# Performance work log

Measured on AMD Instinct MI355X. Metric: run time of the kernel, lower is better.

## Reference

```python
import jax, jax.numpy as jnp
import numpy as np

N, E, D, H, G, L, EF = 50000, 800000, 128, 256, 512, 3, 8
BN_EPS = 1e-5


def _bn(h, g, b):
    # torch BatchNorm1d in training mode: biased batch stats over the node axis
    m = h.mean(0)
    v = h.var(0)
    return g * (h - m) * jax.lax.rsqrt(v + BN_EPS) + b


def setup_inputs() -> dict:
    ks = jax.random.split(jax.random.key(0), 12)
    sc = 0.05
    return {
        "x": jax.random.normal(ks[0], (N, D), jnp.float32),
        "edge_attr": jax.random.normal(ks[1], (E, EF), jnp.float32),
        "vn_emb": jnp.zeros((1, D), jnp.float32),  # init.constant_(0)
        "We": jax.random.normal(ks[2], (L, EF, D)) * sc,
        "be": jnp.zeros((L, D)),
        "W1": jax.random.normal(ks[3], (L, D, H)) * sc,
        "b1": jnp.zeros((L, H)),
        "g1": jnp.ones((L, H)),
        "bt1": jnp.zeros((L, H)),
        "W2": jax.random.normal(ks[4], (L, H, D)) * sc,
        "b2": jnp.zeros((L, D)),
        "gb": jnp.ones((L, D)),
        "bb": jnp.zeros((L, D)),
        "Wv1": jax.random.normal(ks[5], (L - 1, D, H)) * sc,
        "bv1": jnp.zeros((L - 1, H)),
        "gv1": jnp.ones((L - 1, H)),
        "btv1": jnp.zeros((L - 1, H)),
        "Wv2": jax.random.normal(ks[6], (L - 1, H, D)) * sc,
        "bv2": jnp.zeros((L - 1, D)),
        "gv2": jnp.ones((L - 1, D)),
        "btv2": jnp.zeros((L - 1, D)),
        "edge_index": jax.random.randint(ks[7], (2, E), 0, N),
        "batch": jnp.sort(jax.random.randint(ks[8], (N,), 0, G)),
    }


def reference(x, edge_attr, vn_emb, We, be, W1, b1, g1, bt1, W2, b2, gb, bb,
              Wv1, bv1, gv1, btv1, Wv2, bv2, gv2, btv2, edge_index, batch):
    src, dst = edge_index[0], edge_index[1]
    vn = jnp.broadcast_to(vn_emb, (G, D))  # Embedding(1, D) looked up for every graph
    h = x  # node_encoder is None -> encoded_node = x
    for l in range(L):
        h_in = h + vn[batch]                              # virtual-node broadcast (gather)
        e = edge_attr @ We[l] + be[l]                     # per-layer edge encoder
        msg = jax.nn.relu(h_in[src] + e)                  # GIN message, [E, D]
        aggr = jax.ops.segment_sum(msg, dst, num_segments=N)
        z = h_in + aggr                                   # (1+eps)*h + aggr, eps=0
        z = jax.nn.relu(_bn(z @ W1[l] + b1[l], g1[l], bt1[l]))
        h = _bn(z @ W2[l] + b2[l], gb[l], bb[l])          # conv MLP out + outer BatchNorm
        if l < L - 1:
            h = jax.nn.relu(h)                            # dropout ratio 0 -> identity
            pooled = jax.ops.segment_sum(h_in, batch, num_segments=G) + vn
            t = jax.nn.relu(_bn(pooled @ Wv1[l] + bv1[l], gv1[l], btv1[l]))
            vn = jax.nn.relu(_bn(t @ Wv2[l] + bv2[l], gv2[l], btv2[l]))
    return h  # JK == 'last'
```

## Files before the change

kernel.cpp:

```cpp
#include <hip/hip_runtime.h>
#include <hip/hip_bf16.h>

#define N_NODES 50000
#define N_EDGES 800000
#define DIM 128
#define HID 256
#define N_GRAPH 512
#define N_LAYER 3
#define EFEAT 8
#define BN_EPS 1e-5f

typedef unsigned short u16;
typedef unsigned int u32;

using bf16x8_t = short __attribute__((ext_vector_type(8)));
using f32x4_t  = float __attribute__((ext_vector_type(4)));
using f32x2    = float __attribute__((ext_vector_type(2)));


__device__ __forceinline__ void atomic_add_f(float* p, float v) {
    unsafeAtomicAdd(p, v);
}
__device__ __forceinline__ u16 f2bf(float x) {
    union { float f; u32 u; } v; v.f = x;
    u32 r = v.u + 0x7FFF + ((v.u >> 16) & 1);
    return (u16)(r >> 16);
}
__device__ __forceinline__ float bf2f(u16 u) {
    union { u32 i; float f; } v; v.i = (u32)u << 16; return v.f;
}
__device__ __forceinline__ float2 up2(u32 p) {
    return make_float2(bf2f((u16)(p & 0xFFFF)), bf2f((u16)(p >> 16)));
}
__device__ __forceinline__ u32 pk2(float a, float b) {
    return (u32)f2bf(a) | ((u32)f2bf(b) << 16);
}
__device__ __forceinline__ float bflo(u32 u) {
    union { u32 i; float f; } v; v.i = u << 16; return v.f;
}
__device__ __forceinline__ float bfhi(u32 u) {
    union { u32 i; float f; } v; v.i = u & 0xFFFF0000u; return v.f;
}
__device__ __forceinline__ f32x2 up2p(u32 p) {
    union { u32 u[2]; f32x2 f; } v;
    v.u[0] = p << 16;
    v.u[1] = p & 0xFFFF0000u;
    return v.f;
}
__device__ __forceinline__ f32x2 splat2(float x) {
    f32x2 r; r.x = x; r.y = x; return r;
}

__global__ __launch_bounds__(256) void wconv_kernel(
    const float* __restrict__ W1, const float* __restrict__ W2,
    u16* __restrict__ W1t, u16* __restrict__ W2t)
{
    int idx = blockIdx.x * 256 + threadIdx.x;
    if (idx >= 6 * 32768) return;
    int m = idx >> 15;
    int off = idx & 32767;
    int l = m >> 1;
    if ((m & 1) == 0) {
        int r = off >> 8, c = off & 255;
        W1t[(size_t)l * 32768 + c * 128 + r] = f2bf(W1[(size_t)l * 32768 + r * 256 + c]);
    } else {
        int r = off >> 7, c = off & 127;
        W2t[(size_t)l * 32768 + c * 256 + r] = f2bf(W2[(size_t)l * 32768 + r * 128 + c]);
    }
}

__global__ __launch_bounds__(256) void hist_kernel(const int* __restrict__ ei, int* __restrict__ deg) {
    int e = blockIdx.x * 256 + threadIdx.x;
    if (e < N_EDGES) atomicAdd(&deg[ei[N_EDGES + e]], 1);
}

__global__ __launch_bounds__(1024) void scan_kernel(const int* __restrict__ deg, int* __restrict__ rowptr) {
    __shared__ int wsum[16];
    __shared__ int carry;
    int tid = threadIdx.x;
    if (tid == 0) { carry = 0; rowptr[0] = 0; }
    __syncthreads();
    for (int base = 0; base < N_NODES; base += 1024) {
        int i = base + tid;
        int v = (i < N_NODES) ? deg[i] : 0;
        int lane = tid & 63, w = tid >> 6;
        int s = v;
        #pragma unroll
        for (int d = 1; d < 64; d <<= 1) { int t = __shfl_up(s, d); if (lane >= d) s += t; }
        if (lane == 63) wsum[w] = s;
        __syncthreads();
        if (tid < 64) {
            int t = (tid < 16) ? wsum[tid] : 0;
            #pragma unroll
            for (int d = 1; d < 16; d <<= 1) { int u = __shfl_up(t, d); if (tid >= d) t += u; }
            if (tid < 16) wsum[tid] = t;
        }
        __syncthreads();
        int excl = (w > 0) ? wsum[w - 1] : 0;
        int incl = s + excl + carry;
        if (i < N_NODES) rowptr[i + 1] = incl;
        __syncthreads();
        if (tid == 0) carry += wsum[15];
        __syncthreads();
    }
}

__global__ __launch_bounds__(256) void scatter_kernel(
    const int* __restrict__ ei, const float* __restrict__ ea,
    const int* __restrict__ rowptr,
    int* __restrict__ cursor, u32* __restrict__ srcOff, uint4* __restrict__ eabs)
{
    int e = blockIdx.x * 256 + threadIdx.x;
    if (e >= N_EDGES) return;
    int src = ei[e];
    int dst = ei[N_EDGES + e];
    int p = atomicAdd(&cursor[dst], 1);
    int pos = rowptr[dst] + p;
    srcOff[pos] = (u32)src << 8;
    const float4 lo = *(const float4*)(ea + (size_t)e * EFEAT);
    const float4 hi = *(const float4*)(ea + (size_t)e * EFEAT + 4);
    uint4 q;
    q.x = pk2(lo.x, lo.y); q.y = pk2(lo.z, lo.w);
    q.z = pk2(hi.x, hi.y); q.w = pk2(hi.z, hi.w);
    eabs[pos] = q;
}

template <bool USEBN, int VNM>
__global__ __launch_bounds__(256) void hin_kernel(
    const float* __restrict__ src,
    const float* __restrict__ sum2, const float* __restrict__ ss2,
    const float* __restrict__ g, const float* __restrict__ b, float invN,
    const int* __restrict__ batch,
    const float* __restrict__ vn_emb,
    const float* __restrict__ vnpre, const float* __restrict__ vsum, const float* __restrict__ vss,
    const float* __restrict__ gv, const float* __restrict__ btv, float invG,
    u16* __restrict__ hin, int total4)
{
    int idx = blockIdx.x * 256 + threadIdx.x;
    if (idx >= total4) return;
    int base = idx * 4;
    int n = base >> 7;
    int c = base & (DIM - 1);
    float4 v = *(const float4*)(src + base);
    float o[4] = {v.x, v.y, v.z, v.w};
    if (USEBN) {
        #pragma unroll
        for (int j = 0; j < 4; ++j) {
            int cj = c + j;
            float m = sum2[cj] * invN;
            float var = ss2[cj] * invN - m * m;
            float r = rsqrtf(var + BN_EPS);
            float a = g[cj] * r;
            o[j] = fmaxf(fmaf(a, o[j], b[cj] - m * a), 0.f);
        }
    }
    int grp = batch[n];
    if (VNM == 0) {
        const float4 w = *(const float4*)(vn_emb + c);
        o[0] += w.x; o[1] += w.y; o[2] += w.z; o[3] += w.w;
    } else {
        const float4 vp = *(const float4*)(vnpre + (size_t)grp * DIM + c);
        float vv[4] = {vp.x, vp.y, vp.z, vp.w};
        #pragma unroll
        for (int j = 0; j < 4; ++j) {
            int cj = c + j;
            float m = vsum[cj] * invG;
            float var = vss[cj] * invG - m * m;
            float r = rsqrtf(var + BN_EPS);
            float a = gv[cj] * r;
            o[j] += fmaxf(fmaf(a, vv[j], btv[cj] - m * a), 0.f);
        }
    }
    uint2 pk;
    pk.x = pk2(o[0], o[1]);
    pk.y = pk2(o[2], o[3]);
    *(uint2*)(hin + base) = pk;
}

__device__ __forceinline__ void edge_term2(
    u32 h, uint4 eq, const f32x2* rW, f32x2 rB, f32x2& acc)
{
    f32x2 ex = rB;
    ex = __builtin_elementwise_fma(splat2(bflo(eq.x)), rW[0], ex);
    ex = __builtin_elementwise_fma(splat2(bfhi(eq.x)), rW[1], ex);
    ex = __builtin_elementwise_fma(splat2(bflo(eq.y)), rW[2], ex);
    ex = __builtin_elementwise_fma(splat2(bfhi(eq.y)), rW[3], ex);
    ex = __builtin_elementwise_fma(splat2(bflo(eq.z)), rW[4], ex);
    ex = __builtin_elementwise_fma(splat2(bfhi(eq.z)), rW[5], ex);
    ex = __builtin_elementwise_fma(splat2(bflo(eq.w)), rW[6], ex);
    ex = __builtin_elementwise_fma(splat2(bfhi(eq.w)), rW[7], ex);
    f32x2 s = up2p(h) + ex;
    s = __builtin_elementwise_max(s, splat2(0.f));
    acc += s;
}

__global__ __launch_bounds__(256) void aggr_kernel(
    const int* __restrict__ rowptr, const u32* __restrict__ srcOff,
    const uint4* __restrict__ eabs,
    const float* __restrict__ Wel, const float* __restrict__ bel,
    const u16* __restrict__ hin, u16* __restrict__ z, int nWaves)
{
    const int lane = threadIdx.x & 63;
    const int cb = lane * 4;
    const int wid0 = (blockIdx.x << 2) + (threadIdx.x >> 6);

    f32x2 rW[EFEAT];
    #pragma unroll
    for (int k = 0; k < EFEAT; ++k) {
        float2 t = *(const float2*)(Wel + k * DIM + lane * 2);
        rW[k].x = t.x; rW[k].y = t.y;
    }
    float2 tb = *(const float2*)(bel + lane * 2);
    f32x2 rB; rB.x = tb.x; rB.y = tb.y;

    const char* hinB = (const char*)hin;

    for (int node = __builtin_amdgcn_readfirstlane(wid0); node < N_NODES; node += nWaves) {
        int beg = rowptr[node];
        int end = rowptr[node + 1];
        f32x2 acc = up2p(*(const u32*)(hinB + ((u32)node << 8) + cb));

        int i = beg;
        while (i < end && (i & 3)) {
            u32 so = srcOff[i];
            uint4 e0 = eabs[i];
            u32 h0 = *(const u32*)(hinB + so + cb);
            edge_term2(h0, e0, rW, rB, acc);
            ++i;
        }
        for (; i + 3 < end; i += 4) {
            uint4 so4 = *(const uint4*)(srcOff + i);
            uint4 e0 = eabs[i];
            uint4 e1 = eabs[i + 1];
            uint4 e2 = eabs[i + 2];
            uint4 e3 = eabs[i + 3];
            u32 h0 = *(const u32*)(hinB + so4.x + cb);
            u32 h1 = *(const u32*)(hinB + so4.y + cb);
            u32 h2 = *(const u32*)(hinB + so4.z + cb);
            u32 h3 = *(const u32*)(hinB + so4.w + cb);
            edge_term2(h0, e0, rW, rB, acc);
            edge_term2(h1, e1, rW, rB, acc);
            edge_term2(h2, e2, rW, rB, acc);
            edge_term2(h3, e3, rW, rB, acc);
        }
        for (; i < end; ++i) {
            u32 so = srcOff[i];
            uint4 e0 = eabs[i];
            u32 h0 = *(const u32*)(hinB + so + cb);
            edge_term2(h0, e0, rW, rB, acc);
        }
        *(u32*)(z + ((size_t)node << 7) + lane * 2) = pk2(acc.x, acc.y);
    }
}

template <int MODE, bool CBF16>
__global__ __launch_bounds__(256) void gemm_bf16_kernel(
    const u16* __restrict__ Aa,
    const float* __restrict__ sSum, const float* __restrict__ sSS,
    const float* __restrict__ gA, const float* __restrict__ btA, float invCnt,
    const u16* __restrict__ Bt,
    const float* __restrict__ bias,
    void* __restrict__ CoutV,
    float* __restrict__ outSum, float* __restrict__ outSS,
    int M, int K, int Nc)
{
    constexpr int BM = 128, BN = 128, BK = 128;
    constexpr int LDA = BK + 8;
    __shared__ u16 As[BM * LDA];
    __shared__ u16 Bs[64 * LDA];
    __shared__ float csum[BN], css[BN];

    const int tid = threadIdx.x;
    const int wave = tid >> 6, lane = tid & 63;
    const int row0 = blockIdx.x * BM, col0 = blockIdx.y * BN;
    const int w_m = (wave & 1) * 64, w_n = (wave >> 1) * 32;
    const int quad = lane >> 4, l16 = lane & 15;

    if (tid < BN) { csum[tid] = 0.f; css[tid] = 0.f; }

    f32x4_t acc[4][4];
    #pragma unroll
    for (int mi = 0; mi < 4; ++mi)
        #pragma unroll
        for (int ni = 0; ni < 4; ++ni)
            acc[mi][ni] = (f32x4_t){0.f, 0.f, 0.f, 0.f};

    const int kc = (tid & 15) * 8;
    const int nkt = K / BK;

    for (int kt = 0; kt < nkt; ++kt) {
        float af[8], bf_[8];
        if (MODE == 1) {
            #pragma unroll
            for (int j = 0; j < 8; ++j) {
                int kg = kt * BK + kc + j;
                float m = sSum[kg] * invCnt;
                float var = sSS[kg] * invCnt - m * m;
                float r = rsqrtf(var + BN_EPS);
                float a = gA[kg] * r;
                af[j] = a;
                bf_[j] = btA[kg] - m * a;
            }
        }
        #pragma unroll
        for (int it = 0; it < 8; ++it) {
            int chunk = it * 256 + tid;
            int row = chunk >> 4;
            int gr = row0 + row; if (gr >= M) gr = M - 1;
            uint4 q = *(const uint4*)(Aa + (size_t)gr * K + kt * BK + kc);
            if (MODE == 1) {
                float2 p0 = up2(q.x), p1 = up2(q.y), p2 = up2(q.z), p3 = up2(q.w);
                p0.x = fmaxf(fmaf(af[0], p0.x, bf_[0]), 0.f);
                p0.y = fmaxf(fmaf(af[1], p0.y, bf_[1]), 0.f);
                p1.x = fmaxf(fmaf(af[2], p1.x, bf_[2]), 0.f);
                p1.y = fmaxf(fmaf(af[3], p1.y, bf_[3]), 0.f);
                p2.x = fmaxf(fmaf(af[4], p2.x, bf_[4]), 0.f);
                p2.y = fmaxf(fmaf(af[5], p2.y, bf_[5]), 0.f);
                p3.x = fmaxf(fmaf(af[6], p3.x, bf_[6]), 0.f);
                p3.y = fmaxf(fmaf(af[7], p3.y, bf_[7]), 0.f);
                q.x = pk2(p0.x, p0.y); q.y = pk2(p1.x, p1.y);
                q.z = pk2(p2.x, p2.y); q.w = pk2(p3.x, p3.y);
            }
            *(uint4*)(As + row * LDA + kc) = q;
        }
        #pragma unroll
        for (int half = 0; half < 2; ++half) {
            #pragma unroll
            for (int it = 0; it < 4; ++it) {
                int chunk = it * 256 + tid;
                int n = chunk >> 4;
                uint4 q = *(const uint4*)(Bt + (size_t)(col0 + half * 64 + n) * K + kt * BK + kc);
                *(uint4*)(Bs + n * LDA + kc) = q;
            }
            __syncthreads();
            #pragma unroll
            for (int ks = 0; ks < 4; ++ks) {
                bf16x8_t a_frag[4], b_frag[2];
                #pragma unroll
                for (int mi = 0; mi < 4; ++mi)
                    a_frag[mi] = *(const bf16x8_t*)(As + (w_m + mi * 16 + l16) * LDA + ks * 32 + quad * 8);
                #pragma unroll
                for (int ni = 0; ni < 2; ++ni)
                    b_frag[ni] = *(const bf16x8_t*)(Bs + (w_n + ni * 16 + l16) * LDA + ks * 32 + quad * 8);
                #pragma unroll
                for (int mi = 0; mi < 4; ++mi)
                    #pragma unroll
                    for (int ni = 0; ni < 2; ++ni)
                        acc[mi][half * 2 + ni] = __builtin_amdgcn_mfma_f32_16x16x32_bf16(
                            a_frag[mi], b_frag[ni], acc[mi][half * 2 + ni], 0, 0, 0);
            }
            __syncthreads();
        }
    }

    u16* Cb = (u16*)CoutV;
    float* Cf = (float*)CoutV;
    #pragma unroll
    for (int half = 0; half < 2; ++half)
    #pragma unroll
    for (int ni = 0; ni < 2; ++ni) {
        int ccol = half * 64 + w_n + ni * 16 + l16;
        int col = col0 + ccol;
        float bv = bias[col];
        float s = 0.f, qs = 0.f;
        #pragma unroll
        for (int mi = 0; mi < 4; ++mi) {
            int rbase = row0 + w_m + mi * 16 + quad * 4;
            #pragma unroll
            for (int reg = 0; reg < 4; ++reg) {
                int gr = rbase + reg;
                if (gr < M) {
                    float o = acc[mi][half * 2 + ni][reg] + bv;
                    s += o;
                    qs += o * o;
                    if (CBF16) Cb[(size_t)gr * Nc + col] = f2bf(o);
                    else       Cf[(size_t)gr * Nc + col] = o;
                }
            }
        }
        s += __shfl_xor(s, 16);  s += __shfl_xor(s, 32);
        qs += __shfl_xor(qs, 16);  qs += __shfl_xor(qs, 32);
        if (quad == 0) {
            atomicAdd(&csum[ccol], s);
            atomicAdd(&css[ccol], qs);
        }
    }
    __syncthreads();
    if (tid < BN) {
        atomic_add_f(outSum + col0 + tid, csum[tid]);
        atomic_add_f(outSS + col0 + tid, css[tid]);
    }
}

template <int MODE>
__global__ __launch_bounds__(256) void gemm_kernel(
    const float* __restrict__ Aa,
    const float* __restrict__ sSum, const float* __restrict__ sSS,
    const float* __restrict__ gA, const float* __restrict__ btA, float invCnt,
    const float* __restrict__ B, const float* __restrict__ bias,
    float* __restrict__ Cout, float* __restrict__ outSum, float* __restrict__ outSS,
    int M, int K, int Nc)
{
    __shared__ float As[16][68];
    __shared__ float Bs[16][64];
    __shared__ float alphaS[256], betaS[256];
    __shared__ float csum[64], css[64];

    const int tid = threadIdx.x;
    const int tx = tid & 15, ty = tid >> 4;
    const int row0 = blockIdx.x * 64, col0 = blockIdx.y * 64;

    if (tid < 64) { csum[tid] = 0.f; css[tid] = 0.f; }
    if (MODE == 1) {
        for (int k = tid; k < K; k += 256) {
            float m = sSum[k] * invCnt;
            float var = sSS[k] * invCnt - m * m;
            float r = rsqrtf(var + BN_EPS);
            float a = gA[k] * r;
            alphaS[k] = a;
            betaS[k] = btA[k] - m * a;
        }
    }
    __syncthreads();

    float acc[4][4];
    #pragma unroll
    for (int i = 0; i < 4; ++i)
        #pragma unroll
        for (int j = 0; j < 4; ++j) acc[i][j] = 0.f;

    const int lr = tid >> 2;
    const int lk = (tid & 3) * 4;
    const int bk = tid >> 4;
    const int bc = tx * 4;

    for (int kt = 0; kt < K; kt += 16) {
        int gr = row0 + lr;
        float4 va = make_float4(0.f, 0.f, 0.f, 0.f);
        if (gr < M) {
            va = *(const float4*)(Aa + (size_t)gr * K + kt + lk);
            if (MODE == 1) {
                int k0 = kt + lk;
                va.x = fmaxf(fmaf(alphaS[k0 + 0], va.x, betaS[k0 + 0]), 0.f);
                va.y = fmaxf(fmaf(alphaS[k0 + 1], va.y, betaS[k0 + 1]), 0.f);
                va.z = fmaxf(fmaf(alphaS[k0 + 2], va.z, betaS[k0 + 2]), 0.f);
                va.w = fmaxf(fmaf(alphaS[k0 + 3], va.w, betaS[k0 + 3]), 0.f);
            }
        }
        As[lk + 0][lr] = va.x;
        As[lk + 1][lr] = va.y;
        As[lk + 2][lr] = va.z;
        As[lk + 3][lr] = va.w;
        const float4 vb4 = *(const float4*)(B + (size_t)(kt + bk) * Nc + col0 + bc);
        *(float4*)&Bs[bk][bc] = vb4;
        __syncthreads();
        #pragma unroll
        for (int kk = 0; kk < 16; ++kk) {
            const float4 a4 = *(const float4*)&As[kk][ty * 4];
            const float4 b4 = *(const float4*)&Bs[kk][tx * 4];
            float av[4] = {a4.x, a4.y, a4.z, a4.w};
            float bv4[4] = {b4.x, b4.y, b4.z, b4.w};
            #pragma unroll
            for (int i = 0; i < 4; ++i)
                #pragma unroll
                for (int j = 0; j < 4; ++j)
                    acc[i][j] = fmaf(av[i], bv4[j], acc[i][j]);
        }
        __syncthreads();
    }

    const float4 bvv = *(const float4*)(bias + col0 + tx * 4);
    float bias4[4] = {bvv.x, bvv.y, bvv.z, bvv.w};
    float ps[4] = {0.f, 0.f, 0.f, 0.f};
    float pq[4] = {0.f, 0.f, 0.f, 0.f};
    #pragma unroll
    for (int i = 0; i < 4; ++i) {
        int gr = row0 + ty * 4 + i;
        if (gr < M) {
            float o[4];
            #pragma unroll
            for (int j = 0; j < 4; ++j) {
                o[j] = acc[i][j] + bias4[j];
                ps[j] += o[j];
                pq[j] += o[j] * o[j];
            }
            *(float4*)(Cout + (size_t)gr * Nc + col0 + tx * 4) = make_float4(o[0], o[1], o[2], o[3]);
        }
    }
    #pragma unroll
    for (int j = 0; j < 4; ++j) {
        atomicAdd(&csum[tx * 4 + j], ps[j]);
        atomicAdd(&css[tx * 4 + j], pq[j]);
    }
    __syncthreads();
    if (tid < 64) {
        atomic_add_f(outSum + col0 + tid, csum[tid]);
        atomic_add_f(outSS + col0 + tid, css[tid]);
    }
}

template <int VNM>
__global__ __launch_bounds__(128) void pooled_seg_kernel(
    const u16* __restrict__ hin, const int* __restrict__ batch,
    const float* __restrict__ vn_emb,
    const float* __restrict__ vnpre, const float* __restrict__ vsum, const float* __restrict__ vss,
    const float* __restrict__ gv, const float* __restrict__ btv, float invG,
    float* __restrict__ pooled)
{
    int g = blockIdx.x;
    int c = threadIdx.x;
    int lo = 0, hi = N_NODES;
    while (lo < hi) { int mid = (lo + hi) >> 1; if (batch[mid] < g) lo = mid + 1; else hi = mid; }
    int start = lo;
    hi = N_NODES;
    while (lo < hi) { int mid = (lo + hi) >> 1; if (batch[mid] < g + 1) lo = mid + 1; else hi = mid; }
    int end = lo;
    float acc;
    if (VNM == 0) {
        acc = vn_emb[c];
    } else {
        float m = vsum[c] * invG;
        float var = vss[c] * invG - m * m;
        float r = rsqrtf(var + BN_EPS);
        float a = gv[c] * r;
        acc = fmaxf(fmaf(a, vnpre[(size_t)g * DIM + c], btv[c] - m * a), 0.f);
    }
    for (int n = start; n < end; ++n) acc += bf2f(hin[(size_t)n * DIM + c]);
    pooled[(size_t)g * DIM + c] = acc;
}

__global__ __launch_bounds__(256) void final_bn_kernel(
    float* __restrict__ outp, const float* __restrict__ sum2, const float* __restrict__ ss2,
    const float* __restrict__ g, const float* __restrict__ b, float invN, int total4)
{
    int idx = blockIdx.x * 256 + threadIdx.x;
    if (idx >= total4) return;
    int base = idx * 4;
    int c = base & (DIM - 1);
    float4 v = *(const float4*)(outp + base);
    float o[4] = {v.x, v.y, v.z, v.w};
    #pragma unroll
    for (int j = 0; j < 4; ++j) {
        int cj = c + j;
        float m = sum2[cj] * invN;
        float var = ss2[cj] * invN - m * m;
        float r = rsqrtf(var + BN_EPS);
        float a = g[cj] * r;
        o[j] = fmaf(a, o[j], b[cj] - m * a);
    }
    *(float4*)(outp + base) = make_float4(o[0], o[1], o[2], o[3]);
}

extern "C" void kernel_launch(void* const* d_in, const int* in_sizes, int n_in,
                              void* d_out, int out_size, void* d_ws, size_t ws_size,
                              hipStream_t stream) {
    const float* x         = (const float*)d_in[0];
    const float* edge_attr = (const float*)d_in[1];
    const float* vn_emb    = (const float*)d_in[2];
    const float* We        = (const float*)d_in[3];
    const float* be        = (const float*)d_in[4];
    const float* W1        = (const float*)d_in[5];
    const float* b1        = (const float*)d_in[6];
    const float* g1v       = (const float*)d_in[7];
    const float* bt1       = (const float*)d_in[8];
    const float* W2        = (const float*)d_in[9];
    const float* b2        = (const float*)d_in[10];
    const float* gb        = (const float*)d_in[11];
    const float* bb        = (const float*)d_in[12];
    const float* Wv1       = (const float*)d_in[13];
    const float* bv1       = (const float*)d_in[14];
    const float* gv1       = (const float*)d_in[15];
    const float* btv1      = (const float*)d_in[16];
    const float* Wv2       = (const float*)d_in[17];
    const float* bv2       = (const float*)d_in[18];
    const float* gv2       = (const float*)d_in[19];
    const float* btv2      = (const float*)d_in[20];
    const int* edge_index  = (const int*)d_in[21];
    const int* batch       = (const int*)d_in[22];
    float* outp = (float*)d_out;

    auto au = [](size_t x) { return (x + 255) & ~(size_t)255; };
    char* p = (char*)d_ws;
    u16* h_in   = (u16*)p;  p += au((size_t)N_NODES * DIM * 2);
    u16* z_bf   = (u16*)p;  p += au((size_t)N_NODES * DIM * 2);
    u16* c1_bf  = (u16*)p;  p += au((size_t)N_NODES * HID * 2);
    u16* W1t    = (u16*)p;  p += au((size_t)3 * 32768 * 2);
    u16* W2t    = (u16*)p;  p += au((size_t)3 * 32768 * 2);
    float* pooled = (float*)p;  p += au((size_t)N_GRAPH * DIM * 4);
    float* tpre   = (float*)p;  p += au((size_t)N_GRAPH * HID * 4);
    float* vnpre  = (float*)p;  p += au((size_t)N_GRAPH * DIM * 4);
    float* stats  = (float*)p;  p += au(2048 * 4);
    float* sum1 = stats,        *ss1 = stats + 256;
    float* sum2 = stats + 512,  *ss2 = stats + 640;
    float* vsum1 = stats + 768, *vss1 = stats + 1024;
    float* vsum2 = stats + 1280, *vss2 = stats + 1408;
    int* rowptr = (int*)p;  p += au((size_t)(N_NODES + 1) * 4);
    int* cursor = (int*)p;  p += au((size_t)N_NODES * 4);
    u32* srcOff = (u32*)p;  p += au((size_t)N_EDGES * 4);
    uint4* eabs = (uint4*)p;

    const float invN = 1.0f / (float)N_NODES;
    const float invG = 1.0f / (float)N_GRAPH;
    const int total4 = N_NODES * DIM / 4;

    hipMemsetAsync(cursor, 0, N_NODES * sizeof(int), stream);
    hist_kernel<<<(N_EDGES + 255) / 256, 256, 0, stream>>>(edge_index, cursor);
    scan_kernel<<<1, 1024, 0, stream>>>(cursor, rowptr);
    hipMemsetAsync(cursor, 0, N_NODES * sizeof(int), stream);
    scatter_kernel<<<(N_EDGES + 255) / 256, 256, 0, stream>>>(
        edge_index, edge_attr, rowptr, cursor, srcOff, eabs);
    wconv_kernel<<<768, 256, 0, stream>>>(W1, W2, W1t, W2t);

    const int AGGR_BLOCKS = 2048;
    const int nWaves = AGGR_BLOCKS * 4;

    for (int l = 0; l < N_LAYER; ++l) {
        if (l == 0)
            hin_kernel<false, 0><<<(total4 + 255) / 256, 256, 0, stream>>>(
                x, nullptr, nullptr, nullptr, nullptr, 0.f, batch,
                vn_emb, nullptr, nullptr, nullptr, nullptr, nullptr, 0.f,
                h_in, total4);
        else
            hin_kernel<true, 1><<<(total4 + 255) / 256, 256, 0, stream>>>(
                outp, sum2, ss2, gb + (size_t)(l - 1) * DIM, bb + (size_t)(l - 1) * DIM, invN, batch,
                nullptr, vnpre, vsum2, vss2,
                gv2 + (size_t)(l - 1) * DIM, btv2 + (size_t)(l - 1) * DIM, invG,
                h_in, total4);

        if (l == 0)
            pooled_seg_kernel<0><<<N_GRAPH, 128, 0, stream>>>(
                h_in, batch, vn_emb, nullptr, nullptr, nullptr, nullptr, nullptr, 0.f, pooled);
        else if (l < N_LAYER - 1)
            pooled_seg_kernel<1><<<N_GRAPH, 128, 0, stream>>>(
                h_in, batch, nullptr, vnpre, vsum2, vss2,
                gv2 + (size_t)(l - 1) * DIM, btv2 + (size_t)(l - 1) * DIM, invG, pooled);

        hipMemsetAsync(stats, 0, 2048 * sizeof(float), stream);

        aggr_kernel<<<AGGR_BLOCKS, 256, 0, stream>>>(
            rowptr, srcOff, eabs, We + (size_t)l * EFEAT * DIM, be + (size_t)l * DIM,
            h_in, z_bf, nWaves);

        dim3 g1d((N_NODES + 127) / 128, HID / 128);
        gemm_bf16_kernel<0, true><<<g1d, 256, 0, stream>>>(
            z_bf, nullptr, nullptr, nullptr, nullptr, 0.f,
            W1t + (size_t)l * 32768, b1 + (size_t)l * HID,
            (void*)c1_bf, sum1, ss1, N_NODES, DIM, HID);

        dim3 g2d((N_NODES + 127) / 128, DIM / 128);
        gemm_bf16_kernel<1, false><<<g2d, 256, 0, stream>>>(
            c1_bf, sum1, ss1, g1v + (size_t)l * HID, bt1 + (size_t)l * HID, invN,
            W2t + (size_t)l * 32768, b2 + (size_t)l * DIM,
            (void*)outp, sum2, ss2, N_NODES, HID, DIM);

        if (l < N_LAYER - 1) {
            dim3 g3d(N_GRAPH / 64, HID / 64);
            gemm_kernel<0><<<g3d, 256, 0, stream>>>(
                pooled, nullptr, nullptr, nullptr, nullptr, 0.f,
                Wv1 + (size_t)l * DIM * HID, bv1 + (size_t)l * HID,
                tpre, vsum1, vss1, N_GRAPH, DIM, HID);

            dim3 g4d(N_GRAPH / 64, DIM / 64);
            gemm_kernel<1><<<g4d, 256, 0, stream>>>(
                tpre, vsum1, vss1, gv1 + (size_t)l * HID, btv1 + (size_t)l * HID, invG,
                Wv2 + (size_t)l * HID * DIM, bv2 + (size_t)l * DIM,
                vnpre, vsum2, vss2, N_GRAPH, HID, DIM);
        }
    }

    final_bn_kernel<<<(total4 + 255) / 256, 256, 0, stream>>>(
        outp, sum2, ss2, gb + (size_t)2 * DIM, bb + (size_t)2 * DIM, invN, total4);
}
```

Measured before the change: 824.8 us.

## Interleave edge records, reuse histogram ranks in scatter, unroll pooled segment sum

Edge attributes and source offsets are packed into one padded 32-byte record per CSR slot, so the aggregation loop reads a single contiguous stream instead of two arrays. The histogram kernel now records each edge's atomic rank, which lets the scatter skip a second atomic pass and a memset, and it uses nontemporal loads. The pooled segment sum is split across four independent accumulators to expose more parallel loads. The padding raises edge-record traffic from 20 to 32 bytes per edge, and a rank array must now be written and read.

After: 775.5 us. -6.0%, faster.

```diff
diff --git a/kernel.cpp b/kernel.cpp
--- a/kernel.cpp
+++ b/kernel.cpp
@@ -16,6 +16,7 @@
 using bf16x8_t = short __attribute__((ext_vector_type(8)));
 using f32x4_t  = float __attribute__((ext_vector_type(4)));
 using f32x2    = float __attribute__((ext_vector_type(2)));
+using f32x4v   = float __attribute__((ext_vector_type(4)));
 
 
 __device__ __forceinline__ void atomic_add_f(float* p, float v) {
@@ -69,9 +70,13 @@
     }
 }
 
-__global__ __launch_bounds__(256) void hist_kernel(const int* __restrict__ ei, int* __restrict__ deg) {
+__global__ __launch_bounds__(256) void hist_rank_kernel(
+    const int* __restrict__ ei, int* __restrict__ deg, int* __restrict__ rank)
+{
     int e = blockIdx.x * 256 + threadIdx.x;
-    if (e < N_EDGES) atomicAdd(&deg[ei[N_EDGES + e]], 1);
+    if (e >= N_EDGES) return;
+    int dst = ei[N_EDGES + e];
+    rank[e] = atomicAdd(&deg[dst], 1);
 }
 
 __global__ __launch_bounds__(1024) void scan_kernel(const int* __restrict__ deg, int* __restrict__ rowptr) {
@@ -107,22 +112,23 @@
 
 __global__ __launch_bounds__(256) void scatter_kernel(
     const int* __restrict__ ei, const float* __restrict__ ea,
-    const int* __restrict__ rowptr,
-    int* __restrict__ cursor, u32* __restrict__ srcOff, uint4* __restrict__ eabs)
+    const int* __restrict__ rank, const int* __restrict__ rowptr,
+    char* __restrict__ rec)
 {
     int e = blockIdx.x * 256 + threadIdx.x;
     if (e >= N_EDGES) return;
-    int src = ei[e];
-    int dst = ei[N_EDGES + e];
-    int p = atomicAdd(&cursor[dst], 1);
-    int pos = rowptr[dst] + p;
-    srcOff[pos] = (u32)src << 8;
-    const float4 lo = *(const float4*)(ea + (size_t)e * EFEAT);
-    const float4 hi = *(const float4*)(ea + (size_t)e * EFEAT + 4);
+    int src = __builtin_nontemporal_load(ei + e);
+    int dst = __builtin_nontemporal_load(ei + N_EDGES + e);
+    int rk  = __builtin_nontemporal_load(rank + e);
+    int pos = rowptr[dst] + rk;
+    f32x4v lo = __builtin_nontemporal_load((const f32x4v*)(ea + (size_t)e * EFEAT));
+    f32x4v hi = __builtin_nontemporal_load((const f32x4v*)(ea + (size_t)e * EFEAT + 4));
     uint4 q;
     q.x = pk2(lo.x, lo.y); q.y = pk2(lo.z, lo.w);
     q.z = pk2(hi.x, hi.y); q.w = pk2(hi.z, hi.w);
-    eabs[pos] = q;
+    char* rb = rec + ((size_t)pos << 5);
+    *(uint4*)rb = q;
+    *(u32*)(rb + 16) = (u32)src << 8;
 }
 
 template <bool USEBN, int VNM>
@@ -195,8 +201,7 @@
 }
 
 __global__ __launch_bounds__(256) void aggr_kernel(
-    const int* __restrict__ rowptr, const u32* __restrict__ srcOff,
-    const uint4* __restrict__ eabs,
+    const int* __restrict__ rowptr, const char* __restrict__ rec,
     const float* __restrict__ Wel, const float* __restrict__ bel,
     const u16* __restrict__ hin, u16* __restrict__ z, int nWaves)
 {
@@ -220,33 +225,30 @@
         int end = rowptr[node + 1];
         f32x2 acc = up2p(*(const u32*)(hinB + ((u32)node << 8) + cb));
 
+        const char* rb = rec + ((size_t)beg << 5);
         int i = beg;
-        while (i < end && (i & 3)) {
-            u32 so = srcOff[i];
-            uint4 e0 = eabs[i];
-            u32 h0 = *(const u32*)(hinB + so + cb);
-            edge_term2(h0, e0, rW, rB, acc);
-            ++i;
-        }
-        for (; i + 3 < end; i += 4) {
-            uint4 so4 = *(const uint4*)(srcOff + i);
-            uint4 e0 = eabs[i];
-            uint4 e1 = eabs[i + 1];
-            uint4 e2 = eabs[i + 2];
-            uint4 e3 = eabs[i + 3];
-            u32 h0 = *(const u32*)(hinB + so4.x + cb);
-            u32 h1 = *(const u32*)(hinB + so4.y + cb);
-            u32 h2 = *(const u32*)(hinB + so4.z + cb);
-            u32 h3 = *(const u32*)(hinB + so4.w + cb);
+        for (; i + 3 < end; i += 4, rb += 128) {
+            uint4 e0 = *(const uint4*)(rb);
+            u32  s0 = *(const u32*)(rb + 16);
+            uint4 e1 = *(const uint4*)(rb + 32);
+            u32  s1 = *(const u32*)(rb + 48);
+            uint4 e2 = *(const uint4*)(rb + 64);
+            u32  s2 = *(const u32*)(rb + 80);
+            uint4 e3 = *(const uint4*)(rb + 96);
+            u32  s3 = *(const u32*)(rb + 112);
+            u32 h0 = *(const u32*)(hinB + s0 + cb);
+            u32 h1 = *(const u32*)(hinB + s1 + cb);
+            u32 h2 = *(const u32*)(hinB + s2 + cb);
+            u32 h3 = *(const u32*)(hinB + s3 + cb);
             edge_term2(h0, e0, rW, rB, acc);
             edge_term2(h1, e1, rW, rB, acc);
             edge_term2(h2, e2, rW, rB, acc);
             edge_term2(h3, e3, rW, rB, acc);
         }
-        for (; i < end; ++i) {
-            u32 so = srcOff[i];
-            uint4 e0 = eabs[i];
-            u32 h0 = *(const u32*)(hinB + so + cb);
+        for (; i < end; ++i, rb += 32) {
+            uint4 e0 = *(const uint4*)(rb);
+            u32  s0 = *(const u32*)(rb + 16);
+            u32 h0 = *(const u32*)(hinB + s0 + cb);
             edge_term2(h0, e0, rW, rB, acc);
         }
         *(u32*)(z + ((size_t)node << 7) + lane * 2) = pk2(acc.x, acc.y);
@@ -525,7 +527,16 @@
         float a = gv[c] * r;
         acc = fmaxf(fmaf(a, vnpre[(size_t)g * DIM + c], btv[c] - m * a), 0.f);
     }
-    for (int n = start; n < end; ++n) acc += bf2f(hin[(size_t)n * DIM + c]);
+    float a0 = 0.f, a1 = 0.f, a2 = 0.f, a3 = 0.f;
+    int n = start;
+    for (; n + 3 < end; n += 4) {
+        a0 += bf2f(hin[(size_t)(n + 0) * DIM + c]);
+        a1 += bf2f(hin[(size_t)(n + 1) * DIM + c]);
+        a2 += bf2f(hin[(size_t)(n + 2) * DIM + c]);
+        a3 += bf2f(hin[(size_t)(n + 3) * DIM + c]);
+    }
+    for (; n < end; ++n) a0 += bf2f(hin[(size_t)n * DIM + c]);
+    acc += (a0 + a1) + (a2 + a3);
     pooled[(size_t)g * DIM + c] = acc;
 }
 
@@ -595,20 +606,19 @@
     float* vsum1 = stats + 768, *vss1 = stats + 1024;
     float* vsum2 = stats + 1280, *vss2 = stats + 1408;
     int* rowptr = (int*)p;  p += au((size_t)(N_NODES + 1) * 4);
-    int* cursor = (int*)p;  p += au((size_t)N_NODES * 4);
-    u32* srcOff = (u32*)p;  p += au((size_t)N_EDGES * 4);
-    uint4* eabs = (uint4*)p;
+    int* deg    = (int*)p;  p += au((size_t)N_NODES * 4);
+    int* rank   = (int*)p;  p += au((size_t)N_EDGES * 4);
+    char* rec   = p;
 
     const float invN = 1.0f / (float)N_NODES;
     const float invG = 1.0f / (float)N_GRAPH;
     const int total4 = N_NODES * DIM / 4;
 
-    hipMemsetAsync(cursor, 0, N_NODES * sizeof(int), stream);
-    hist_kernel<<<(N_EDGES + 255) / 256, 256, 0, stream>>>(edge_index, cursor);
-    scan_kernel<<<1, 1024, 0, stream>>>(cursor, rowptr);
-    hipMemsetAsync(cursor, 0, N_NODES * sizeof(int), stream);
+    hipMemsetAsync(deg, 0, N_NODES * sizeof(int), stream);
+    hist_rank_kernel<<<(N_EDGES + 255) / 256, 256, 0, stream>>>(edge_index, deg, rank);
+    scan_kernel<<<1, 1024, 0, stream>>>(deg, rowptr);
     scatter_kernel<<<(N_EDGES + 255) / 256, 256, 0, stream>>>(
-        edge_index, edge_attr, rowptr, cursor, srcOff, eabs);
+        edge_index, edge_attr, rank, rowptr, rec);
     wconv_kernel<<<768, 256, 0, stream>>>(W1, W2, W1t, W2t);
 
     const int AGGR_BLOCKS = 2048;
@@ -638,7 +648,7 @@
         hipMemsetAsync(stats, 0, 2048 * sizeof(float), stream);
 
         aggr_kernel<<<AGGR_BLOCKS, 256, 0, stream>>>(
-            rowptr, srcOff, eabs, We + (size_t)l * EFEAT * DIM, be + (size_t)l * DIM,
+            rowptr, rec, We + (size_t)l * EFEAT * DIM, be + (size_t)l * DIM,
             h_in, z_bf, nWaves);
 
         dim3 g1d((N_NODES + 127) / 128, HID / 128);
```
